# Optimization experiments

Measured on AMD Instinct MI355X. Metric: run time of the kernel, lower is better.

The kernel has to match this reference:

```python
import jax, jax.numpy as jnp
import numpy as np

N_NODES = 100000
N_EDGES = 6400000
DIM_FEAT = 5


def setup_inputs() -> dict:
    key = jax.random.key(0)
    k1, k2, k3 = jax.random.split(key, 3)
    features = jax.random.normal(k1, (N_NODES, DIM_FEAT), dtype=jnp.float32)
    src = jax.random.randint(k2, (N_EDGES,), 0, N_NODES, dtype=jnp.int64)
    dst = jax.random.randint(k3, (N_EDGES,), 0, N_NODES, dtype=jnp.int64)
    return {"features": features, "src": src, "dst": dst}


def reference(features, src, dst):
    # copy_u('h','m') then sum('m','h'):
    # h_out[v] = sum over edges (u->v) of features[u]
    msgs = features[src]  # [E, F] gather
    h = jax.ops.segment_sum(msgs, dst, num_segments=N_NODES)  # [N, F]
    return h
```

## Files before the change

kernel.cpp:

```cpp
#include <hip/hip_runtime.h>
#include <hip/hip_bf16.h>


#define NN     100000
#define FD     5
#define NOUTT  (NN * FD)
#define NPS    32
#define NPS_SH 5
#define NB     3125
#define NSB    512
#define BLK    256

__global__ __launch_bounds__(BLK) void k2_hist(const int* __restrict__ dst,
                                               unsigned short* __restrict__ bh,
                                               int chunk) {
    __shared__ int h[NB];
    for (int b = threadIdx.x; b < NB; b += BLK) h[b] = 0;
    __syncthreads();
    long long e0 = (long long)blockIdx.x * chunk;
    const int4* d4 = (const int4*)(dst + e0);
    int n4 = chunk >> 2;
    for (int i = threadIdx.x; i < n4; i += BLK) {
        int4 d = d4[i];
        atomicAdd(&h[d.x >> NPS_SH], 1);
        atomicAdd(&h[d.y >> NPS_SH], 1);
        atomicAdd(&h[d.z >> NPS_SH], 1);
        atomicAdd(&h[d.w >> NPS_SH], 1);
    }
    __syncthreads();
    unsigned short* row = bh + (size_t)blockIdx.x * NB;
    for (int b = threadIdx.x; b < NB; b += BLK) row[b] = (unsigned short)h[b];
}

__global__ __launch_bounds__(BLK) void k3_scanblk(unsigned short* __restrict__ bh,
                                                  int* __restrict__ btot) {
    __shared__ int s[BLK];
    int b = blockIdx.x, t = threadIdx.x;
    int v0 = bh[(size_t)(2 * t)     * NB + b];
    int v1 = bh[(size_t)(2 * t + 1) * NB + b];
    int pair = v0 + v1;
    s[t] = pair;
    __syncthreads();
    for (int off = 1; off < BLK; off <<= 1) {
        int v = (t >= off) ? s[t - off] : 0;
        __syncthreads();
        s[t] += v;
        __syncthreads();
    }
    int base = s[t] - pair;
    bh[(size_t)(2 * t)     * NB + b] = (unsigned short)base;
    bh[(size_t)(2 * t + 1) * NB + b] = (unsigned short)(base + v0);
    if (t == BLK - 1) btot[b] = s[t];
}

#define VPT 13
__global__ __launch_bounds__(BLK) void k4_scanbkt(const int* __restrict__ btot,
                                                  int* __restrict__ bbase) {
    __shared__ int s[BLK];
    int t = threadIdx.x;
    int v[VPT], sum = 0;
#pragma unroll
    for (int k = 0; k < VPT; ++k) {
        int i = VPT * t + k;
        v[k] = (i < NB) ? btot[i] : 0;
        sum += v[k];
    }
    s[t] = sum;
    __syncthreads();
    for (int off = 1; off < BLK; off <<= 1) {
        int u = (t >= off) ? s[t - off] : 0;
        __syncthreads();
        s[t] += u;
        __syncthreads();
    }
    int run = s[t] - sum;
#pragma unroll
    for (int k = 0; k < VPT; ++k) {
        int i = VPT * t + k;
        if (i < NB) bbase[i] = run;
        run += v[k];
    }
}

__global__ __launch_bounds__(BLK) void k5_scatter(const int* __restrict__ src,
                                                  const int* __restrict__ dst,
                                                  const unsigned short* __restrict__ bh,
                                                  const int* __restrict__ bbase,
                                                  int* __restrict__ bdata, int chunk) {
    __shared__ int cur[NB];
    int blk = blockIdx.x;
    const unsigned short* row = bh + (size_t)blk * NB;
    for (int b = threadIdx.x; b < NB; b += BLK)
        cur[b] = bbase[b] + (int)row[b];
    __syncthreads();
    long long e0 = (long long)blk * chunk;
    const int4* d4 = (const int4*)(dst + e0);
    const int4* s4 = (const int4*)(src + e0);
    int n4 = chunk >> 2;
    for (int i = threadIdx.x; i < n4; i += BLK) {
        int4 d = d4[i];
        int4 s = s4[i];
        int vv[4] = {d.x, d.y, d.z, d.w};
        int uu[4] = {s.x, s.y, s.z, s.w};
#pragma unroll
        for (int j = 0; j < 4; ++j) {
            int b = vv[j] >> NPS_SH;
            int off = atomicAdd(&cur[b], 1);
            bdata[off] = (uu[j] << NPS_SH) | (vv[j] & (NPS - 1));
        }
    }
}

__global__ __launch_bounds__(BLK) void k1_pad(const float* __restrict__ f,
                                              float4* __restrict__ fp) {
    int i = blockIdx.x * BLK + threadIdx.x;
    if (i < NN) {
        const float* r = f + (long long)i * FD;
        fp[2 * i]     = make_float4(r[0], r[1], r[2], r[3]);
        fp[2 * i + 1] = make_float4(r[4], 0.f, 0.f, 0.f);
    }
}

#define UNR 8
__global__ __launch_bounds__(BLK) void k6_gather(const int* __restrict__ bdata,
                                                 const float4* __restrict__ fp,
                                                 const int* __restrict__ bbase,
                                                 const int* __restrict__ btot,
                                                 float* __restrict__ out) {
    __shared__ float acc[NPS * FD];
    int t = threadIdx.x;
    if (t < NPS * FD) acc[t] = 0.f;
    __syncthreads();
    int b = blockIdx.x;
    int base = bbase[b];
    int n = btot[b];
    const float* fpf = (const float*)fp;

    int i = t;
    for (; i + (UNR - 1) * BLK < n; i += UNR * BLK) {
        int    l[UNR];
        float4 a[UNR];
        float  cx[UNR];
#pragma unroll
        for (int k = 0; k < UNR; ++k) {
            int w = bdata[base + i + k * BLK];
            int u = w >> NPS_SH;
            l[k] = w & (NPS - 1);
            a[k] = fp[2 * u];
            cx[k] = fpf[8 * u + 4];
        }
#pragma unroll
        for (int k = 0; k < UNR; ++k) {
            float* p = acc + l[k] * FD;
            atomicAdd(&p[0], a[k].x);
            atomicAdd(&p[1], a[k].y);
            atomicAdd(&p[2], a[k].z);
            atomicAdd(&p[3], a[k].w);
            atomicAdd(&p[4], cx[k]);
        }
    }
    for (; i < n; i += BLK) {
        int w = bdata[base + i];
        int u = w >> NPS_SH;
        int l = w & (NPS - 1);
        float4 a = fp[2 * u];
        float cx = fpf[8 * u + 4];
        float* p = acc + l * FD;
        atomicAdd(&p[0], a.x); atomicAdd(&p[1], a.y); atomicAdd(&p[2], a.z);
        atomicAdd(&p[3], a.w); atomicAdd(&p[4], cx);
    }
    __syncthreads();
    float* o = out + (long long)b * NPS * FD;
    if (t < NPS * FD) o[t] = acc[t];
}

__global__ void scatter_add_fallback(const float* __restrict__ features,
                                     const int* __restrict__ src,
                                     const int* __restrict__ dst,
                                     float* __restrict__ out, int n_edges) {
    int idx = blockIdx.x * blockDim.x + threadIdx.x;
    int stride = gridDim.x * blockDim.x;
    for (int e = idx; e < n_edges; e += stride) {
        int u = src[e], v = dst[e];
        const float* f = features + (long long)u * FD;
        float* o = out + (long long)v * FD;
#pragma unroll
        for (int k = 0; k < FD; ++k) atomicAdd(&o[k], f[k]);
    }
}

extern "C" void kernel_launch(void* const* d_in, const int* in_sizes, int n_in,
                              void* d_out, int out_size, void* d_ws, size_t ws_size,
                              hipStream_t stream) {
    const float* features = (const float*)d_in[0];
    const int*   src      = (const int*)d_in[1];
    const int*   dst      = (const int*)d_in[2];
    float* out = (float*)d_out;
    int n_edges = in_sizes[1];

    size_t o_bd = 0;
    size_t o_bh = o_bd + (size_t)n_edges * 4;
    size_t o_fp = o_bh;
    size_t sz_overlap = (size_t)NSB * NB * 2;
    size_t sz_fp = (size_t)NN * 2 * sizeof(float4);
    if (sz_fp > sz_overlap) sz_overlap = sz_fp;
    size_t o_bb = o_bh + ((sz_overlap + 15) & ~(size_t)15);
    size_t o_bt = o_bb + (size_t)NB * 4;
    size_t need = o_bt + (size_t)NB * 4;

    bool fast = (out_size == NOUTT) && (in_sizes[0] == NOUTT) &&
                (n_edges % (NSB * 4) == 0) && (need <= ws_size);

    if (fast) {
        char* w = (char*)d_ws;
        int*            bdata = (int*)(w + o_bd);
        unsigned short* bhist = (unsigned short*)(w + o_bh);
        float4*         fpad  = (float4*)(w + o_fp);
        int*            bbase = (int*)(w + o_bb);
        int*            btot  = (int*)(w + o_bt);
        int chunk = n_edges / NSB;
        k2_hist  <<<NSB, BLK, 0, stream>>>(dst, bhist, chunk);
        k3_scanblk<<<NB, BLK, 0, stream>>>(bhist, btot);
        k4_scanbkt<<<1,  BLK, 0, stream>>>(btot, bbase);
        k5_scatter<<<NSB, BLK, 0, stream>>>(src, dst, bhist, bbase, bdata, chunk);
        k1_pad   <<<(NN + BLK - 1) / BLK, BLK, 0, stream>>>(features, fpad);
        k6_gather <<<NB,  BLK, 0, stream>>>(bdata, fpad, bbase, btot, out);
    } else {
        hipMemsetAsync(d_out, 0, (size_t)out_size * sizeof(float), stream);
        int grid = (n_edges + BLK - 1) / BLK;
        if (grid > 65535) grid = 65535;
        scatter_add_fallback<<<grid, BLK, 0, stream>>>(features, src, dst, out, n_edges);
    }
}
```

Before: 394.1 us.

## Gather bf16-packed features and split each bucket across two blocks

Features are packed into one 16-byte bf16 record per node instead of two float4s, so each edge gathers a single vector load instead of two. The gather grid is doubled: each of the 3125 output buckets is split between two blocks, which combine their results with global atomics into a pre-zeroed output. A scheduling barrier keeps all loads ahead of the LDS atomics. Rounding features to bf16 adds precision error over roughly 64 accumulated terms per node and may exceed tolerance. The split also adds a memset and global atomics.

```diff
diff --git a/kernel.cpp b/kernel.cpp
--- a/kernel.cpp
+++ b/kernel.cpp
@@ -10,6 +10,14 @@
 #define NB     3125
 #define NSB    512
 #define BLK    256
+
+__device__ inline unsigned bf16rtn(float x) {
+    unsigned u = __float_as_uint(x);
+    u += 0x7fffu + ((u >> 16) & 1u);
+    return u >> 16;
+}
+__device__ inline float lo16(unsigned v) { return __uint_as_float(v << 16); }
+__device__ inline float hi16(unsigned v) { return __uint_as_float(v & 0xffff0000u); }
 
 __global__ __launch_bounds__(BLK) void k2_hist(const int* __restrict__ dst,
                                                unsigned short* __restrict__ bh,
@@ -112,18 +120,24 @@
 }
 
 __global__ __launch_bounds__(BLK) void k1_pad(const float* __restrict__ f,
-                                              float4* __restrict__ fp) {
+                                              uint4* __restrict__ fp) {
     int i = blockIdx.x * BLK + threadIdx.x;
     if (i < NN) {
         const float* r = f + (long long)i * FD;
-        fp[2 * i]     = make_float4(r[0], r[1], r[2], r[3]);
-        fp[2 * i + 1] = make_float4(r[4], 0.f, 0.f, 0.f);
+        unsigned w0 = bf16rtn(r[0]), w1 = bf16rtn(r[1]), w2 = bf16rtn(r[2]);
+        unsigned w3 = bf16rtn(r[3]), w4 = bf16rtn(r[4]);
+        uint4 o;
+        o.x = w0 | (w1 << 16);
+        o.y = w2 | (w3 << 16);
+        o.z = w4;
+        o.w = 0u;
+        fp[i] = o;
     }
 }
 
 #define UNR 8
 __global__ __launch_bounds__(BLK) void k6_gather(const int* __restrict__ bdata,
-                                                 const float4* __restrict__ fp,
+                                                 const uint4* __restrict__ fp,
                                                  const int* __restrict__ bbase,
                                                  const int* __restrict__ btot,
                                                  float* __restrict__ out) {
@@ -131,47 +145,47 @@
     int t = threadIdx.x;
     if (t < NPS * FD) acc[t] = 0.f;
     __syncthreads();
-    int b = blockIdx.x;
+    int bid = blockIdx.x;
+    int b = bid >> 1, r = bid & 1;
     int base = bbase[b];
     int n = btot[b];
-    const float* fpf = (const float*)fp;
+    int n0 = n >> 1;
+    int s0 = base + (r ? n0 : 0);
+    int cnt = r ? (n - n0) : n0;
 
     int i = t;
-    for (; i + (UNR - 1) * BLK < n; i += UNR * BLK) {
-        int    l[UNR];
-        float4 a[UNR];
-        float  cx[UNR];
+    for (; i + (UNR - 1) * BLK < cnt; i += UNR * BLK) {
+        int   l[UNR];
+        uint4 g[UNR];
 #pragma unroll
         for (int k = 0; k < UNR; ++k) {
-            int w = bdata[base + i + k * BLK];
-            int u = w >> NPS_SH;
+            int w = bdata[s0 + i + k * BLK];
             l[k] = w & (NPS - 1);
-            a[k] = fp[2 * u];
-            cx[k] = fpf[8 * u + 4];
+            g[k] = fp[w >> NPS_SH];
         }
+        __builtin_amdgcn_sched_barrier(0);
 #pragma unroll
         for (int k = 0; k < UNR; ++k) {
             float* p = acc + l[k] * FD;
-            atomicAdd(&p[0], a[k].x);
-            atomicAdd(&p[1], a[k].y);
-            atomicAdd(&p[2], a[k].z);
-            atomicAdd(&p[3], a[k].w);
-            atomicAdd(&p[4], cx[k]);
+            atomicAdd(&p[0], lo16(g[k].x));
+            atomicAdd(&p[1], hi16(g[k].x));
+            atomicAdd(&p[2], lo16(g[k].y));
+            atomicAdd(&p[3], hi16(g[k].y));
+            atomicAdd(&p[4], lo16(g[k].z));
         }
     }
-    for (; i < n; i += BLK) {
-        int w = bdata[base + i];
-        int u = w >> NPS_SH;
+    for (; i < cnt; i += BLK) {
+        int w = bdata[s0 + i];
         int l = w & (NPS - 1);
-        float4 a = fp[2 * u];
-        float cx = fpf[8 * u + 4];
+        uint4 g = fp[w >> NPS_SH];
         float* p = acc + l * FD;
-        atomicAdd(&p[0], a.x); atomicAdd(&p[1], a.y); atomicAdd(&p[2], a.z);
-        atomicAdd(&p[3], a.w); atomicAdd(&p[4], cx);
-    }
-    __syncthreads();
-    float* o = out + (long long)b * NPS * FD;
-    if (t < NPS * FD) o[t] = acc[t];
+        atomicAdd(&p[0], lo16(g.x)); atomicAdd(&p[1], hi16(g.x));
+        atomicAdd(&p[2], lo16(g.y)); atomicAdd(&p[3], hi16(g.y));
+        atomicAdd(&p[4], lo16(g.z));
+    }
+    __syncthreads();
+    if (t < NPS * FD)
+        atomicAdd(&out[(size_t)b * NPS * FD + t], acc[t]);
 }
 
 __global__ void scatter_add_fallback(const float* __restrict__ features,
@@ -202,7 +216,7 @@
     size_t o_bh = o_bd + (size_t)n_edges * 4;
     size_t o_fp = o_bh;
     size_t sz_overlap = (size_t)NSB * NB * 2;
-    size_t sz_fp = (size_t)NN * 2 * sizeof(float4);
+    size_t sz_fp = (size_t)NN * sizeof(uint4);
     if (sz_fp > sz_overlap) sz_overlap = sz_fp;
     size_t o_bb = o_bh + ((sz_overlap + 15) & ~(size_t)15);
     size_t o_bt = o_bb + (size_t)NB * 4;
@@ -215,16 +229,17 @@
         char* w = (char*)d_ws;
         int*            bdata = (int*)(w + o_bd);
         unsigned short* bhist = (unsigned short*)(w + o_bh);
-        float4*         fpad  = (float4*)(w + o_fp);
+        uint4*          fpad  = (uint4*)(w + o_fp);
         int*            bbase = (int*)(w + o_bb);
         int*            btot  = (int*)(w + o_bt);
         int chunk = n_edges / NSB;
+        hipMemsetAsync(d_out, 0, (size_t)out_size * sizeof(float), stream);
         k2_hist  <<<NSB, BLK, 0, stream>>>(dst, bhist, chunk);
         k3_scanblk<<<NB, BLK, 0, stream>>>(bhist, btot);
         k4_scanbkt<<<1,  BLK, 0, stream>>>(btot, bbase);
         k5_scatter<<<NSB, BLK, 0, stream>>>(src, dst, bhist, bbase, bdata, chunk);
         k1_pad   <<<(NN + BLK - 1) / BLK, BLK, 0, stream>>>(features, fpad);
-        k6_gather <<<NB,  BLK, 0, stream>>>(bdata, fpad, bbase, btot, out);
+        k6_gather <<<2 * NB, BLK, 0, stream>>>(bdata, fpad, bbase, btot, out);
     } else {
         hipMemsetAsync(d_out, 0, (size_t)out_size * sizeof(float), stream);
         int grid = (n_edges + BLK - 1) / BLK;
```

Measured after the change: 395.6 us. No clear change (+0.4%).
